# Kernel optimization log

Measured on AMD Instinct MI355X. Metric: run time of the kernel, lower is better.

The kernel has to match this reference:

```python
import jax, jax.numpy as jnp
import numpy as np

B, L, D, H, V, NBARS = 128, 256, 256, 256, 130, 17


def _lstm(x, h, c, Wih, Whh, bih, bhh):
    # torch nn.LSTMCell math
    g = x @ Wih.T + h @ Whh.T + (bih + bhh)
    i, f, gg, o = jnp.split(g, 4, axis=-1)
    c2 = jax.nn.sigmoid(f) * c + jax.nn.sigmoid(i) * jnp.tanh(gg)
    return jax.nn.sigmoid(o) * jnp.tanh(c2), c2


def setup_inputs() -> dict:
    key = jax.random.key(0)
    ks = jax.random.split(key, 10)
    s = 0.05
    return dict(
        c=jax.random.normal(ks[0], (B, NBARS, D), jnp.float32),
        target=jax.random.randint(ks[1], (3, B, L), 0, V),
        length=L,
        W_hid=jax.random.normal(ks[2], (2 * D, D), jnp.float32) * s,
        b_hid=jnp.zeros((2 * D,), jnp.float32),
        W1_ih=jax.random.normal(ks[3], (3, 4 * H, 2 * D), jnp.float32) * s,
        W1_hh=jax.random.normal(ks[4], (3, 4 * H, H), jnp.float32) * s,
        b1_ih=jnp.zeros((3, 4 * H), jnp.float32),
        b1_hh=jnp.zeros((3, 4 * H), jnp.float32),
        Wc_ih=jax.random.normal(ks[5], (4 * H, 3 * H), jnp.float32) * s,
        Wc_hh=jax.random.normal(ks[6], (4 * H, H), jnp.float32) * s,
        bc_ih=jnp.zeros((4 * H,), jnp.float32),
        bc_hh=jnp.zeros((4 * H,), jnp.float32),
        emb=jax.random.normal(ks[7], (3, V, D), jnp.float32) * s,
        Wout=jax.random.normal(ks[8], (3, V, H), jnp.float32) * s,
        bout=jnp.zeros((3, V), jnp.float32),
    )


def _forward(c, W_hid, b_hid, W1_ih, W1_hh, b1_ih, b1_hh, Wc_ih, Wc_hh,
             bc_ih, bc_hh, emb, Wout, bout, target, length):
    Bsz = c.shape[0]
    # initial notes: embedding of token 0 for each of the 3 streams
    notes0 = jnp.broadcast_to(emb[:, 0, :][:, None, :], (3, Bsz, D))
    z3 = jnp.zeros((3, Bsz, H), c.dtype)
    z1 = jnp.zeros((Bsz, H), c.dtype)
    carry0 = (z3, z3, z3, z3, z1, z1, notes0)

    def step(carry, t):
        h1, c1, h2, c2, hc, cc, notes = carry
        bar = t // 16
        c_bar = jax.lax.dynamic_index_in_dim(c, bar, axis=1, keepdims=False)      # [B, D]
        c_t = jax.lax.dynamic_index_in_dim(c, bar + 1, axis=1, keepdims=False)    # [B, D]
        h_init = jnp.tanh(c_bar @ W_hid.T + b_hid)[:, :H]
        reset = (t % 16) == 0
        rs = lambda x: jnp.where(reset, jnp.broadcast_to(h_init, x.shape), x)
        zr = lambda x: jnp.where(reset, jnp.zeros_like(x), x)
        h1, c1, h2, c2, hc, cc = rs(h1), zr(c1), rs(h2), zr(c2), rs(hc), zr(cc)

        # first lstm1 update for all 3 streams (independent -> vmap)
        c_t3 = jnp.broadcast_to(c_t, (3,) + c_t.shape)
        x1 = jnp.concatenate([notes, c_t3], axis=-1)                               # [3, B, 2D]
        h1, c1 = jax.vmap(_lstm)(x1, h1, c1, W1_ih, W1_hh, b1_ih, b1_hh)

        tgt = jax.lax.dynamic_index_in_dim(target, t, axis=2, keepdims=False)      # [3, B]
        h1l = [h1[i] for i in range(3)]
        c1l = [c1[i] for i in range(3)]
        h2l = [h2[i] for i in range(3)]
        c2l = [c2[i] for i in range(3)]
        nl = [notes[i] for i in range(3)]
        outs = []
        # sequential dependency through the context cell -> small fixed loop of 3
        for i in range(3):
            hc, cc = _lstm(jnp.concatenate(h1l, axis=-1), hc, cc, Wc_ih, Wc_hh, bc_ih, bc_hh)
            h2l[i], c2l[i] = _lstm(jnp.concatenate([hc, c_t], axis=-1), h2l[i], c2l[i],
                                   W1_ih[i], W1_hh[i], b1_ih[i], b1_hh[i])
            outs.append((h1l[i] + h2l[i]) @ Wout[i].T + bout[i])                   # [B, V]
            nl[i] = emb[i][tgt[i]]                                                 # teacher forcing
            h1l[i], c1l[i] = _lstm(jnp.concatenate([nl[i], c_t], axis=-1), h1l[i], c1l[i],
                                   W1_ih[i], W1_hh[i], b1_ih[i], b1_hh[i])
        carry = (jnp.stack(h1l), jnp.stack(c1l), jnp.stack(h2l), jnp.stack(c2l),
                 hc, cc, jnp.stack(nl))
        return carry, jnp.stack(outs)                                              # [3, B, V]

    _, ys = jax.lax.scan(step, carry0, jnp.arange(length))                         # [L, 3, B, V]
    return jnp.transpose(ys, (1, 2, 0, 3))                                         # [3, B, L, V]


def reference(c, target, length, W_hid, b_hid, W1_ih, W1_hh, b1_ih, b1_hh,
              Wc_ih, Wc_hh, bc_ih, bc_hh, emb, Wout, bout):
    return _forward(c, W_hid, b_hid, W1_ih, W1_hh, b1_ih, b1_hh, Wc_ih, Wc_hh,
                    bc_ih, bc_hh, emb, Wout, bout, target, length)
```

## Files before the change

### kernel.cpp

```cpp
#include <hip/hip_runtime.h>
#include <hip/hip_bf16.h>

typedef float  f32x4  __attribute__((ext_vector_type(4)));
typedef short  short8 __attribute__((ext_vector_type(8)));
typedef short  bf4    __attribute__((ext_vector_type(4)));

#define MFMA16(a,b,c) __builtin_amdgcn_mfma_f32_16x16x32_bf16((a),(b),(c),0,0,0)

__device__ __forceinline__ short tobf(float f){
  unsigned u = __float_as_uint(f);
  u += 0x7fffu + ((u >> 16) & 1u);
  return (short)(u >> 16);
}
__device__ __forceinline__ float frombf(short s){
  return __uint_as_float(((unsigned)(unsigned short)s) << 16);
}
__device__ __forceinline__ float sigf(float x){
  return 1.f / (1.f + __expf(-x));
}
__device__ __forceinline__ float tanhf_(float x){
  float ax = fabsf(x);
  float e  = __expf(-2.f * ax);
  float t  = (1.f - e) / (1.f + e);
  return x >= 0.f ? t : -t;
}
__device__ __forceinline__ bf4 pack4(f32x4 v){
  bf4 r; r[0]=tobf(v[0]); r[1]=tobf(v[1]); r[2]=tobf(v[2]); r[3]=tobf(v[3]); return r;
}

__device__ __forceinline__ int hoff(int row, int col){
  return (row*512 + col*2) ^ ((row & 7) << 4);
}
__device__ __forceinline__ void stH(short* buf, int row, int col, short v){
  *(short*)((char*)buf + hoff(row,col)) = v;
}
__device__ __forceinline__ short8 ldA(const short* buf, int k0, int lane){
  int row = lane & 15;
  int off = (row*512 + (k0 + ((lane>>4)<<3))*2) ^ ((row & 7) << 4);
  return *(const short8*)((const char*)buf + off);
}
__device__ __forceinline__ short* cpPtr(short* cp, int s, int w, int g, int lane){
  return cp + (((s*16 + w)*4 + g) << 8) + (lane << 2);
}
__device__ __forceinline__ f32x4 ldCP(const short* cp, int s, int w, int g, int lane){
  bf4 v = *(const bf4*)(cp + (((s*16 + w)*4 + g) << 8) + (lane << 2));
  f32x4 r; r[0]=frombf(v[0]); r[1]=frombf(v[1]); r[2]=frombf(v[2]); r[3]=frombf(v[3]);
  return r;
}
__device__ __forceinline__ f32x4 ldCS(const float* b, int sl, int tid){
  return *(const f32x4*)(b + sl*4096 + tid*4);
}
__device__ __forceinline__ void stCS(float* b, int sl, int tid, f32x4 v){
  *(f32x4*)(b + sl*4096 + tid*4) = v;
}

__device__ __forceinline__ void gemm256(f32x4 (&acc)[4], const short* __restrict__ W,
                                        int KT, int kt0, const short* __restrict__ A,
                                        int lane, int w){
  const short* w0 = W + (((     w)*KT + kt0)*64 + lane)*8;
  const short* w1 = W + (((16 + w)*KT + kt0)*64 + lane)*8;
  const short* w2 = W + (((32 + w)*KT + kt0)*64 + lane)*8;
  const short* w3 = W + (((48 + w)*KT + kt0)*64 + lane)*8;
  short8 b0[4], b1[4], b2[4], b3[4];
#define GLD(B,K) do{ (B)[0]=*(const short8*)(w0+(K)*512); (B)[1]=*(const short8*)(w1+(K)*512); \
                     (B)[2]=*(const short8*)(w2+(K)*512); (B)[3]=*(const short8*)(w3+(K)*512);}while(0)
#define GMM(B,K) do{ short8 a0_=ldA(A,(K)*32,lane); \
  acc[0]=MFMA16(a0_,(B)[0],acc[0]); acc[1]=MFMA16(a0_,(B)[1],acc[1]); \
  acc[2]=MFMA16(a0_,(B)[2],acc[2]); acc[3]=MFMA16(a0_,(B)[3],acc[3]);}while(0)
  GLD(b0,0); GLD(b1,1); GLD(b2,2); GLD(b3,3);
  GMM(b0,0); GLD(b0,4);
  GMM(b1,1); GLD(b1,5);
  GMM(b2,2); GLD(b2,6);
  GMM(b3,3); GLD(b3,7);
  GMM(b0,4);
  GMM(b1,5);
  GMM(b2,6);
  GMM(b3,7);
#undef GLD
#undef GMM
}

__device__ __forceinline__ void gemm256_dual(f32x4 (&acc)[4], f32x4 (&dacc)[4],
                                             const short* __restrict__ W,
                                             const short* __restrict__ A1,
                                             const short* __restrict__ A2,
                                             int lane, int w){
  const short* w0 = W + ((     w)*8*64 + lane)*8;
  const short* w1 = W + ((16 + w)*8*64 + lane)*8;
  const short* w2 = W + ((32 + w)*8*64 + lane)*8;
  const short* w3 = W + ((48 + w)*8*64 + lane)*8;
  short8 b0[4], b1[4];
#define DLD2(B,K) do{ (B)[0]=*(const short8*)(w0+(K)*512); (B)[1]=*(const short8*)(w1+(K)*512); \
                      (B)[2]=*(const short8*)(w2+(K)*512); (B)[3]=*(const short8*)(w3+(K)*512);}while(0)
#define DMM2(B,K) do{ short8 a1_=ldA(A1,(K)*32,lane); short8 a2_=ldA(A2,(K)*32,lane); \
  acc[0]=MFMA16(a1_,(B)[0],acc[0]);  dacc[0]=MFMA16(a2_,(B)[0],dacc[0]); \
  acc[1]=MFMA16(a1_,(B)[1],acc[1]);  dacc[1]=MFMA16(a2_,(B)[1],dacc[1]); \
  acc[2]=MFMA16(a1_,(B)[2],acc[2]);  dacc[2]=MFMA16(a2_,(B)[2],dacc[2]); \
  acc[3]=MFMA16(a1_,(B)[3],acc[3]);  dacc[3]=MFMA16(a2_,(B)[3],dacc[3]);}while(0)
  DLD2(b0,0); DLD2(b1,1);
  DMM2(b0,0); DLD2(b0,2);
  DMM2(b1,1); DLD2(b1,3);
  DMM2(b0,2); DLD2(b0,4);
  DMM2(b1,3); DLD2(b1,5);
  DMM2(b0,4); DLD2(b0,6);
  DMM2(b1,5); DLD2(b1,7);
  DMM2(b0,6);
  DMM2(b1,7);
#undef DLD2
#undef DMM2
}

__global__ void swz_kernel(short* __restrict__ dst, const float* __restrict__ src,
                           int rowStride, int colOff, int Nreal,
                           int KTtot, int kt0, int ktN, int NT){
  int idx = blockIdx.x*256 + threadIdx.x;
  if (idx >= NT*ktN*512) return;
  int j = idx & 7, l = (idx>>3) & 63, tile = idx >> 9;
  int nt = tile / ktN, ktl = tile - nt*ktN;
  int n = nt*16 + (l & 15);
  int k = ktl*32 + ((l>>4)<<3) + j;
  float v = (n < Nreal) ? src[n*rowStride + colOff + k] : 0.f;
  dst[(((nt*KTtot + kt0 + ktl)*64 + l)<<3) + j] = tobf(v);
}

__global__ __launch_bounds__(1024) void eproj_kernel(
    const float* __restrict__ emb, const float* __restrict__ b1_ih,
    const float* __restrict__ b1_hh, const short* __restrict__ W1ihA_s,
    short* __restrict__ eprojb){
  __shared__ short es[36864];
  const int s = blockIdx.x;
  const int tid = threadIdx.x, lane = tid & 63, w = tid >> 6;
  const int l15 = lane & 15, lg = lane >> 4;
  for (int idx = tid; idx < 36864; idx += 1024){
    int row = idx >> 8, c2 = idx & 255;
    float v = (row < 130) ? emb[(s*130 + row)*256 + c2] : 0.f;
    *(short*)((char*)es + ((row*512 + c2*2) ^ ((row & 7) << 4))) = tobf(v);
  }
  __syncthreads();
  f32x4 z4 = {0.f,0.f,0.f,0.f};
  for (int rt = 0; rt < 9; ++rt){
    const short* Arow = es + rt*4096;
    f32x4 acc[4] = {z4, z4, z4, z4};
    #pragma unroll 2
    for (int kt = 0; kt < 8; ++kt){
      short8 a = ldA(Arow, kt*32, lane);
      #pragma unroll
      for (int q = 0; q < 4; ++q){
        short8 b = *(const short8*)(W1ihA_s + s*262144 + (((w*4+q)*8 + kt)*64 + lane)*8);
        acc[q] = MFMA16(a, b, acc[q]);
      }
    }
    #pragma unroll
    for (int q = 0; q < 4; ++q)
      #pragma unroll
      for (int r = 0; r < 4; ++r){
        int v = rt*16 + lg*4 + r;
        if (v < 130){
          int gc = (w*4 + q)*16 + l15;
          eprojb[(s*130 + v)*1024 + ((gc & 255) << 2) + (gc >> 8)] =
            tobf(acc[q][r] + b1_ih[s*1024 + gc] + b1_hh[s*1024 + gc]);
        }
      }
  }
}

__global__ __launch_bounds__(1024)
__attribute__((amdgpu_waves_per_eu(4,4))) void rnn_main(
    const float* __restrict__ cbuf, const int* __restrict__ tgt,
    const float* __restrict__ b_hid, const float* __restrict__ b1_ih,
    const float* __restrict__ b1_hh, const float* __restrict__ bc_ih,
    const float* __restrict__ bc_hh, const float* __restrict__ boutp,
    const short* __restrict__ eprojb, short* __restrict__ cpart,
    float* __restrict__ cst,
    const short* __restrict__ W1hh_s, const short* __restrict__ W1ihA_s,
    const short* __restrict__ W1ihB_s, const short* __restrict__ Wc_s,
    const short* __restrict__ Whid_s, const short* __restrict__ Wout_s,
    float* __restrict__ outp)
{
  __shared__ short h1b[3*4096];
  __shared__ short h2b[3*4096];
  __shared__ short hcb[4096];

  const int tid  = threadIdx.x;
  const int lane = tid & 63;
  const int w    = tid >> 6;
  const int l15  = lane & 15;
  const int lg   = lane >> 4;
  const int chunk = blockIdx.x;
  const int bar   = blockIdx.y;
  const int b0    = chunk * 16;
  const int cc    = w*16 + l15;
  const int wgid  = bar*8 + chunk;

  short* cpWG  = cpart + wgid*49152;
  float* cstWG = cst + (size_t)wgid*28672;
  const f32x4 z4 = {0.f,0.f,0.f,0.f};

  #pragma unroll 1
  for (int tt = 0; tt < 16; ++tt){
    const int t = bar*16 + tt;

    if (tt == 0){
      for (int idx = tid; idx < 4096; idx += 1024){
        int row = idx >> 8, c2 = idx & 255;
        stH(h2b,        row, c2, tobf(cbuf[((b0+row)*17 + bar)*256 + c2]));
        stH(h2b + 4096, row, c2, tobf(cbuf[((b0+row)*17 + bar + 1)*256 + c2]));
      }
      __syncthreads();
      f32x4 hi0 = z4;
      #pragma unroll
      for (int kt = 0; kt < 8; ++kt){
        short8 a0 = ldA(h2b, kt*32, lane);
        short8 bb = *(const short8*)(Whid_s + ((w*8 + kt)*64 + lane)*8);
        hi0 = MFMA16(a0, bb, hi0);
      }
      #pragma unroll 1
      for (int s = 0; s < 3; ++s){
        f32x4 acc[4] = {z4, z4, z4, z4};
        gemm256(acc, W1ihB_s + s*262144, 8, 0, h2b + 4096, lane, w);
        #pragma unroll
        for (int g = 0; g < 4; ++g)
          *(bf4*)cpPtr(cpWG, s, w, g, lane) = pack4(acc[g]);
      }
      __syncthreads();
      {
        float bh = b_hid[cc];
        #pragma unroll
        for (int r = 0; r < 4; ++r){
          int row = lg*4 + r;
          short hv = tobf(tanhf_(hi0[r] + bh));
          stH(h1b,       row,cc,hv); stH(h1b+4096, row,cc,hv); stH(h1b+8192,row,cc,hv);
          stH(h2b,       row,cc,hv); stH(h2b+4096, row,cc,hv); stH(h2b+8192,row,cc,hv);
          stH(hcb,       row,cc,hv);
        }
      }
      __syncthreads();
    }

    #pragma unroll 1
    for (int s = 0; s < 3; ++s){
      f32x4 cold = tt ? ldCS(cstWG, s, tid) : z4;
      f32x4 acc[4];
      #pragma unroll
      for (int g = 0; g < 4; ++g) acc[g] = ldCP(cpWG, s, w, g, lane);
      gemm256(acc, W1hh_s + s*262144, 8, 0, h1b + s*4096, lane, w);
      __syncthreads();
      f32x4 cnew;
      #pragma unroll
      for (int r = 0; r < 4; ++r){
        const int row = lg*4 + r;
        const int tok = (t == 0) ? 0 : tgt[(s*128 + b0 + row)*256 + (t-1)];
        bf4 e4 = *(const bf4*)(eprojb + (size_t)(s*130 + tok)*1024 + cc*4);
        float pi = acc[0][r] + frombf(e4[0]);
        float pf = acc[1][r] + frombf(e4[1]);
        float pg = acc[2][r] + frombf(e4[2]);
        float po = acc[3][r] + frombf(e4[3]);
        float cs = sigf(pf)*cold[r] + sigf(pi)*tanhf_(pg);
        cnew[r] = cs;
        stH(h1b + s*4096, row, cc, tobf(sigf(po)*tanhf_(cs)));
      }
      stCS(cstWG, s, tid, cnew);
    }
    __syncthreads();

    #pragma unroll 1
    for (int i = 0; i < 3; ++i){
      {
        f32x4 cold = (tt == 0 && i == 0) ? z4 : ldCS(cstWG, 6, tid);
        f32x4 acc[4] = {z4, z4, z4, z4};
        #pragma unroll 1
        for (int seg = 0; seg < 4; ++seg){
          const short* Ax = (seg==0) ? h1b : (seg==1) ? (h1b+4096)
                           : (seg==2) ? (h1b+8192) : hcb;
          gemm256(acc, Wc_s, 32, seg*8, Ax, lane, w);
        }
        __syncthreads();
        const float bi = bc_ih[cc]      + bc_hh[cc];
        const float bf = bc_ih[256+cc]  + bc_hh[256+cc];
        const float bg = bc_ih[512+cc]  + bc_hh[512+cc];
        const float bo = bc_ih[768+cc]  + bc_hh[768+cc];
        f32x4 cnew;
        #pragma unroll
        for (int r = 0; r < 4; ++r){
          const int row = lg*4 + r;
          float cs = sigf(acc[1][r] + bf)*cold[r]
                   + sigf(acc[0][r] + bi)*tanhf_(acc[2][r] + bg);
          cnew[r] = cs;
          stH(hcb, row, cc, tobf(sigf(acc[3][r] + bo)*tanhf_(cs)));
        }
        stCS(cstWG, 6, tid, cnew);
        __syncthreads();
      }
      f32x4 dacc[4];
      {
        f32x4 cold = (tt == 0) ? z4 : ldCS(cstWG, 3+i, tid);
        f32x4 acc[4];
        #pragma unroll
        for (int g = 0; g < 4; ++g){ acc[g] = ldCP(cpWG, i, w, g, lane); dacc[g] = acc[g]; }
        gemm256(acc, W1ihA_s + i*262144, 8, 0, hcb, lane, w);
        gemm256_dual(acc, dacc, W1hh_s + i*262144, h2b + i*4096, h1b + i*4096, lane, w);
        __syncthreads();
        const float bi = b1_ih[i*1024+cc]      + b1_hh[i*1024+cc];
        const float bf = b1_ih[i*1024+256+cc]  + b1_hh[i*1024+256+cc];
        const float bg = b1_ih[i*1024+512+cc]  + b1_hh[i*1024+512+cc];
        const float bo = b1_ih[i*1024+768+cc]  + b1_hh[i*1024+768+cc];
        f32x4 cnew;
        #pragma unroll
        for (int r = 0; r < 4; ++r){
          const int row = lg*4 + r;
          float cs = sigf(acc[1][r] + bf)*cold[r]
                   + sigf(acc[0][r] + bi)*tanhf_(acc[2][r] + bg);
          cnew[r] = cs;
          stH(h2b + i*4096, row, cc, tobf(sigf(acc[3][r] + bo)*tanhf_(cs)));
        }
        stCS(cstWG, 3+i, tid, cnew);
        __syncthreads();
      }
      {
        f32x4 cold = ldCS(cstWG, i, tid);
        f32x4 e0 = z4;
        const short* h1p = h1b + i*4096;
        const short* h2p = h2b + i*4096;
        if (w < 9){
          const short* wo = Wout_s + i*36864 + ((w*8)*64 + lane)*8;
          short8 ebA = *(const short8*)(wo);
          short8 ebB = *(const short8*)(wo + 512);
#define EMM(EB,K) do{ short8 a_=ldA(h1p,(K)*32,lane), f_=ldA(h2p,(K)*32,lane); \
  e0 = MFMA16(a_,(EB),e0); e0 = MFMA16(f_,(EB),e0); }while(0)
          EMM(ebA,0); ebA = *(const short8*)(wo + 2*512);
          EMM(ebB,1); ebB = *(const short8*)(wo + 3*512);
          EMM(ebA,2); ebA = *(const short8*)(wo + 4*512);
          EMM(ebB,3); ebB = *(const short8*)(wo + 5*512);
          EMM(ebA,4); ebA = *(const short8*)(wo + 6*512);
          EMM(ebB,5); ebB = *(const short8*)(wo + 7*512);
          EMM(ebA,6);
          EMM(ebB,7);
#undef EMM
        }
        __syncthreads();
        f32x4 cnew;
        #pragma unroll
        for (int r = 0; r < 4; ++r){
          const int row = lg*4 + r;
          const int tok = tgt[(i*128 + b0 + row)*256 + t];
          bf4 e4 = *(const bf4*)(eprojb + (size_t)(i*130 + tok)*1024 + cc*4);
          float pi = dacc[0][r] + frombf(e4[0]);
          float pf = dacc[1][r] + frombf(e4[1]);
          float pg = dacc[2][r] + frombf(e4[2]);
          float po = dacc[3][r] + frombf(e4[3]);
          float cs = sigf(pf)*cold[r] + sigf(pi)*tanhf_(pg);
          cnew[r] = cs;
          stH(h1b + i*4096, row, cc, tobf(sigf(po)*tanhf_(cs)));
        }
        stCS(cstWG, i, tid, cnew);
        if (w < 8){
          const int v = w*16 + l15;
          const float bo = boutp[i*130 + v];
          #pragma unroll
          for (int r = 0; r < 4; ++r){
            const int row = lg*4 + r;
            outp[(size_t)((i*128 + b0 + row)*256 + t)*130 + v] = e0[r] + bo;
          }
        } else if (w == 8 && l15 < 2){
          const int v = 128 + l15;
          const float bo = boutp[i*130 + v];
          #pragma unroll
          for (int r = 0; r < 4; ++r){
            const int row = lg*4 + r;
            outp[(size_t)((i*128 + b0 + row)*256 + t)*130 + v] = e0[r] + bo;
          }
        }
        __syncthreads();
      }
    }
  }
}

extern "C" void kernel_launch(void* const* d_in, const int* in_sizes, int n_in,
                              void* d_out, int out_size, void* d_ws, size_t ws_size,
                              hipStream_t stream){
  (void)in_sizes; (void)n_in; (void)out_size; (void)ws_size;
  const float* c     = (const float*)d_in[0];
  const int*   tgt   = (const int*)  d_in[1];
  const float* W_hid = (const float*)d_in[3];
  const float* b_hid = (const float*)d_in[4];
  const float* W1_ih = (const float*)d_in[5];
  const float* W1_hh = (const float*)d_in[6];
  const float* b1_ih = (const float*)d_in[7];
  const float* b1_hh = (const float*)d_in[8];
  const float* Wc_ih = (const float*)d_in[9];
  const float* Wc_hh = (const float*)d_in[10];
  const float* bc_ih = (const float*)d_in[11];
  const float* bc_hh = (const float*)d_in[12];
  const float* emb   = (const float*)d_in[13];
  const float* Wout  = (const float*)d_in[14];
  const float* bout  = (const float*)d_in[15];
  float* outp = (float*)d_out;

  short* ws = (short*)d_ws;
  short* W1hh_s  = ws;
  short* W1ihA_s = ws + 786432;
  short* W1ihB_s = ws + 1572864;
  short* Wc_s    = ws + 2359296;
  short* Whid_s  = ws + 3407872;
  short* Wout_s  = ws + 3473408;
  short* eprojb  = ws + 3584000;
  short* cpart   = ws + 3983360;
  float* cstate  = (float*)((char*)d_ws + 20549632);

  for (int s = 0; s < 3; ++s){
    swz_kernel<<<1024,256,0,stream>>>(W1hh_s  + s*262144, W1_hh + s*262144, 256,   0, 1024,  8, 0,  8, 64);
    swz_kernel<<<1024,256,0,stream>>>(W1ihA_s + s*262144, W1_ih + s*524288, 512,   0, 1024,  8, 0,  8, 64);
    swz_kernel<<<1024,256,0,stream>>>(W1ihB_s + s*262144, W1_ih + s*524288, 512, 256, 1024,  8, 0,  8, 64);
    swz_kernel<<< 144,256,0,stream>>>(Wout_s  + s*36864,  Wout  + s*33280,  256,   0,  130,  8, 0,  8,  9);
  }
  swz_kernel<<<3072,256,0,stream>>>(Wc_s,   Wc_ih, 768, 0, 1024, 32,  0, 24, 64);
  swz_kernel<<<1024,256,0,stream>>>(Wc_s,   Wc_hh, 256, 0, 1024, 32, 24,  8, 64);
  swz_kernel<<< 256,256,0,stream>>>(Whid_s, W_hid, 256, 0,  512,  8,  0,  8, 16);
  eproj_kernel<<<3,1024,0,stream>>>(emb, b1_ih, b1_hh, W1ihA_s, eprojb);

  rnn_main<<<dim3(8,16),1024,0,stream>>>(c, tgt, b_hid, b1_ih, b1_hh, bc_ih, bc_hh,
                                         bout, eprojb, cpart, cstate,
                                         W1hh_s, W1ihA_s, W1ihB_s,
                                         Wc_s, Whid_s, Wout_s, outp);
}
```

Baseline: 2.747 ms.

## Stream GEMM weight tiles through LDS with global_load_lds triple buffering

Replaces direct global-to-register weight loads in the recurrent GEMMs with asynchronous global_load_lds transfers into a triple-buffered shared-memory staging area, using manual vmcnt waits. Each wave then reads its weight fragments from LDS. The aim is deeper, asynchronous prefetch of weights with less register pressure. It adds 96KB of LDS, and the hand-written vmcnt counting can interact badly with other outstanding loads.

```diff
diff --git a/kernel.cpp b/kernel.cpp
--- a/kernel.cpp
+++ b/kernel.cpp
@@ -6,6 +6,9 @@
 typedef short  bf4    __attribute__((ext_vector_type(4)));
 
 #define MFMA16(a,b,c) __builtin_amdgcn_mfma_f32_16x16x32_bf16((a),(b),(c),0,0,0)
+#define GLOADLDS(SRC, DST) __builtin_amdgcn_global_load_lds( \
+  (const __attribute__((address_space(1))) void*)(SRC), \
+  (__attribute__((address_space(3))) void*)(DST), 16, 0, 0)
 
 __device__ __forceinline__ short tobf(float f){
   unsigned u = __float_as_uint(f);
@@ -80,34 +83,63 @@
 #undef GMM
 }
 
-__device__ __forceinline__ void gemm256_dual(f32x4 (&acc)[4], f32x4 (&dacc)[4],
-                                             const short* __restrict__ W,
-                                             const short* __restrict__ A1,
-                                             const short* __restrict__ A2,
-                                             int lane, int w){
-  const short* w0 = W + ((     w)*8*64 + lane)*8;
-  const short* w1 = W + ((16 + w)*8*64 + lane)*8;
-  const short* w2 = W + ((32 + w)*8*64 + lane)*8;
-  const short* w3 = W + ((48 + w)*8*64 + lane)*8;
-  short8 b0[4], b1[4];
-#define DLD2(B,K) do{ (B)[0]=*(const short8*)(w0+(K)*512); (B)[1]=*(const short8*)(w1+(K)*512); \
-                      (B)[2]=*(const short8*)(w2+(K)*512); (B)[3]=*(const short8*)(w3+(K)*512);}while(0)
-#define DMM2(B,K) do{ short8 a1_=ldA(A1,(K)*32,lane); short8 a2_=ldA(A2,(K)*32,lane); \
-  acc[0]=MFMA16(a1_,(B)[0],acc[0]);  dacc[0]=MFMA16(a2_,(B)[0],dacc[0]); \
-  acc[1]=MFMA16(a1_,(B)[1],acc[1]);  dacc[1]=MFMA16(a2_,(B)[1],dacc[1]); \
-  acc[2]=MFMA16(a1_,(B)[2],acc[2]);  dacc[2]=MFMA16(a2_,(B)[2],dacc[2]); \
-  acc[3]=MFMA16(a1_,(B)[3],acc[3]);  dacc[3]=MFMA16(a2_,(B)[3],dacc[3]);}while(0)
-  DLD2(b0,0); DLD2(b1,1);
-  DMM2(b0,0); DLD2(b0,2);
-  DMM2(b1,1); DLD2(b1,3);
-  DMM2(b0,2); DLD2(b0,4);
-  DMM2(b1,3); DLD2(b1,5);
-  DMM2(b0,4); DLD2(b0,6);
-  DMM2(b1,5); DLD2(b1,7);
-  DMM2(b0,6);
-  DMM2(b1,7);
-#undef DLD2
-#undef DMM2
+#define HST(B,H) do{ \
+    const int kt_ = kt0 + ((H)>>1); \
+    const int gb_ = ((H)&1)<<1; \
+    GLOADLDS(Wb + ((((gb_    )*16 + w)*KT + kt_) << 9) + (lane<<3), \
+             (char*)wb + (B)*32768 + (w<<11)); \
+    GLOADLDS(Wb + ((((gb_ + 1)*16 + w)*KT + kt_) << 9) + (lane<<3), \
+             (char*)wb + (B)*32768 + (w<<11) + 1024); \
+  }while(0)
+#define WAITH(H) do{ \
+    if ((H) < 14)      { asm volatile("s_waitcnt vmcnt(4)" ::: "memory"); } \
+    else if ((H) == 14){ asm volatile("s_waitcnt vmcnt(2)" ::: "memory"); } \
+    else               { asm volatile("s_waitcnt vmcnt(0)" ::: "memory"); } \
+    __builtin_amdgcn_sched_barrier(0); \
+  }while(0)
+
+__device__ __forceinline__ void gemmL(f32x4 (&acc)[4], const short* __restrict__ Wb,
+                                      int KT, int kt0, const short* __restrict__ A,
+                                      short* wb, int lane, int w){
+  HST(0,0); HST(1,1); HST(2,2);
+  #pragma unroll
+  for (int h = 0; h < 16; ++h){
+    WAITH(h);
+    const int b = h % 3;
+    const char* base = (const char*)wb + b*32768 + (w<<11) + (lane<<4);
+    short8 t0 = *(const short8*)(base);
+    short8 t1 = *(const short8*)(base + 1024);
+    short8 a0_ = ldA(A, (h>>1)*32, lane);
+    const int g0 = (h&1)<<1;
+    acc[g0]   = MFMA16(a0_, t0, acc[g0]);
+    acc[g0+1] = MFMA16(a0_, t1, acc[g0+1]);
+    if (h < 13) HST((h+3)%3, h+3);
+  }
+}
+
+__device__ __forceinline__ void gemmL_dual(f32x4 (&acc)[4], f32x4 (&dacc)[4],
+                                           const short* __restrict__ Wb,
+                                           const short* __restrict__ A1,
+                                           const short* __restrict__ A2,
+                                           short* wb, int lane, int w){
+  const int KT = 8, kt0 = 0;
+  HST(0,0); HST(1,1); HST(2,2);
+  #pragma unroll
+  for (int h = 0; h < 16; ++h){
+    WAITH(h);
+    const int b = h % 3;
+    const char* base = (const char*)wb + b*32768 + (w<<11) + (lane<<4);
+    short8 t0 = *(const short8*)(base);
+    short8 t1 = *(const short8*)(base + 1024);
+    short8 a1_ = ldA(A1, (h>>1)*32, lane);
+    short8 a2_ = ldA(A2, (h>>1)*32, lane);
+    const int g0 = (h&1)<<1;
+    acc[g0]    = MFMA16(a1_, t0, acc[g0]);
+    dacc[g0]   = MFMA16(a2_, t0, dacc[g0]);
+    acc[g0+1]  = MFMA16(a1_, t1, acc[g0+1]);
+    dacc[g0+1] = MFMA16(a2_, t1, dacc[g0+1]);
+    if (h < 13) HST((h+3)%3, h+3);
+  }
 }
 
 __global__ void swz_kernel(short* __restrict__ dst, const float* __restrict__ src,
@@ -180,6 +212,7 @@
   __shared__ short h1b[3*4096];
   __shared__ short h2b[3*4096];
   __shared__ short hcb[4096];
+  __shared__ short wbuf[49152];
 
   const int tid  = threadIdx.x;
   const int lane = tid & 63;
@@ -243,7 +276,7 @@
       f32x4 acc[4];
       #pragma unroll
       for (int g = 0; g < 4; ++g) acc[g] = ldCP(cpWG, s, w, g, lane);
-      gemm256(acc, W1hh_s + s*262144, 8, 0, h1b + s*4096, lane, w);
+      gemmL(acc, W1hh_s + s*262144, 8, 0, h1b + s*4096, wbuf, lane, w);
       __syncthreads();
       f32x4 cnew;
       #pragma unroll
@@ -272,7 +305,7 @@
         for (int seg = 0; seg < 4; ++seg){
           const short* Ax = (seg==0) ? h1b : (seg==1) ? (h1b+4096)
                            : (seg==2) ? (h1b+8192) : hcb;
-          gemm256(acc, Wc_s, 32, seg*8, Ax, lane, w);
+          gemmL(acc, Wc_s, 32, seg*8, Ax, wbuf, lane, w);
         }
         __syncthreads();
         const float bi = bc_ih[cc]      + bc_hh[cc];
@@ -297,8 +330,8 @@
         f32x4 acc[4];
         #pragma unroll
         for (int g = 0; g < 4; ++g){ acc[g] = ldCP(cpWG, i, w, g, lane); dacc[g] = acc[g]; }
-        gemm256(acc, W1ihA_s + i*262144, 8, 0, hcb, lane, w);
-        gemm256_dual(acc, dacc, W1hh_s + i*262144, h2b + i*4096, h1b + i*4096, lane, w);
+        gemmL(acc, W1ihA_s + i*262144, 8, 0, hcb, wbuf, lane, w);
+        gemmL_dual(acc, dacc, W1hh_s + i*262144, h2b + i*4096, h1b + i*4096, wbuf, lane, w);
         __syncthreads();
         const float bi = b1_ih[i*1024+cc]      + b1_hh[i*1024+cc];
         const float bf = b1_ih[i*1024+256+cc]  + b1_hh[i*1024+256+cc];
```

Result: faster. 2.644 ms, median of 3 (-3.7%).

## Stream LSTM weights through LDS with async global_load_lds double buffering

Applied to the files above, without the earlier changes.

Replaces the direct register weight loads in the W1hh, Wc and fused W1ihA/W1hh GEMMs with a pipe2 helper. It issues global_load_lds copies into a double-buffered 64KB LDS region and waits on vmcnt before each consumer step, so weight fetches overlap the MFMAs. Per-bar context partial products now stay in registers as packed bf16 instead of going through a global scratch buffer, and the Wc cell state moves from global memory to shared memory. The cost is higher LDS usage, which may limit occupancy at 1024 threads, and more register pressure from the twelve held bf4 values.

```diff
diff --git a/kernel.cpp b/kernel.cpp
--- a/kernel.cpp
+++ b/kernel.cpp
@@ -6,6 +6,9 @@
 typedef short  bf4    __attribute__((ext_vector_type(4)));
 
 #define MFMA16(a,b,c) __builtin_amdgcn_mfma_f32_16x16x32_bf16((a),(b),(c),0,0,0)
+#define GLOADLDS(SRC, DST) __builtin_amdgcn_global_load_lds( \
+  (const __attribute__((address_space(1))) void*)(SRC), \
+  (__attribute__((address_space(3))) void*)(DST), 16, 0, 0)
 
 __device__ __forceinline__ short tobf(float f){
   unsigned u = __float_as_uint(f);
@@ -27,6 +30,10 @@
 __device__ __forceinline__ bf4 pack4(f32x4 v){
   bf4 r; r[0]=tobf(v[0]); r[1]=tobf(v[1]); r[2]=tobf(v[2]); r[3]=tobf(v[3]); return r;
 }
+__device__ __forceinline__ f32x4 unpack4(bf4 v){
+  f32x4 r; r[0]=frombf(v[0]); r[1]=frombf(v[1]); r[2]=frombf(v[2]); r[3]=frombf(v[3]);
+  return r;
+}
 
 __device__ __forceinline__ int hoff(int row, int col){
   return (row*512 + col*2) ^ ((row & 7) << 4);
@@ -38,14 +45,6 @@
   int row = lane & 15;
   int off = (row*512 + (k0 + ((lane>>4)<<3))*2) ^ ((row & 7) << 4);
   return *(const short8*)((const char*)buf + off);
-}
-__device__ __forceinline__ short* cpPtr(short* cp, int s, int w, int g, int lane){
-  return cp + (((s*16 + w)*4 + g) << 8) + (lane << 2);
-}
-__device__ __forceinline__ f32x4 ldCP(const short* cp, int s, int w, int g, int lane){
-  bf4 v = *(const bf4*)(cp + (((s*16 + w)*4 + g) << 8) + (lane << 2));
-  f32x4 r; r[0]=frombf(v[0]); r[1]=frombf(v[1]); r[2]=frombf(v[2]); r[3]=frombf(v[3]);
-  return r;
 }
 __device__ __forceinline__ f32x4 ldCS(const float* b, int sl, int tid){
   return *(const f32x4*)(b + sl*4096 + tid*4);
@@ -80,34 +79,24 @@
 #undef GMM
 }
 
-__device__ __forceinline__ void gemm256_dual(f32x4 (&acc)[4], f32x4 (&dacc)[4],
-                                             const short* __restrict__ W,
-                                             const short* __restrict__ A1,
-                                             const short* __restrict__ A2,
-                                             int lane, int w){
-  const short* w0 = W + ((     w)*8*64 + lane)*8;
-  const short* w1 = W + ((16 + w)*8*64 + lane)*8;
-  const short* w2 = W + ((32 + w)*8*64 + lane)*8;
-  const short* w3 = W + ((48 + w)*8*64 + lane)*8;
-  short8 b0[4], b1[4];
-#define DLD2(B,K) do{ (B)[0]=*(const short8*)(w0+(K)*512); (B)[1]=*(const short8*)(w1+(K)*512); \
-                      (B)[2]=*(const short8*)(w2+(K)*512); (B)[3]=*(const short8*)(w3+(K)*512);}while(0)
-#define DMM2(B,K) do{ short8 a1_=ldA(A1,(K)*32,lane); short8 a2_=ldA(A2,(K)*32,lane); \
-  acc[0]=MFMA16(a1_,(B)[0],acc[0]);  dacc[0]=MFMA16(a2_,(B)[0],dacc[0]); \
-  acc[1]=MFMA16(a1_,(B)[1],acc[1]);  dacc[1]=MFMA16(a2_,(B)[1],dacc[1]); \
-  acc[2]=MFMA16(a1_,(B)[2],acc[2]);  dacc[2]=MFMA16(a2_,(B)[2],dacc[2]); \
-  acc[3]=MFMA16(a1_,(B)[3],acc[3]);  dacc[3]=MFMA16(a2_,(B)[3],dacc[3]);}while(0)
-  DLD2(b0,0); DLD2(b1,1);
-  DMM2(b0,0); DLD2(b0,2);
-  DMM2(b1,1); DLD2(b1,3);
-  DMM2(b0,2); DLD2(b0,4);
-  DMM2(b1,3); DLD2(b1,5);
-  DMM2(b0,4); DLD2(b0,6);
-  DMM2(b1,5); DLD2(b1,7);
-  DMM2(b0,6);
-  DMM2(b1,7);
-#undef DLD2
-#undef DMM2
+template<int NH, class FS, class FC>
+__device__ __forceinline__ void pipe2(FS fsrc, FC fcons, short* wb, int w, int lane){
+#define STG(B,H) do{ \
+    GLOADLDS(fsrc((H),0) + (lane<<3), (char*)wb + (B)*32768 + (w<<11)); \
+    GLOADLDS(fsrc((H),1) + (lane<<3), (char*)wb + (B)*32768 + (w<<11) + 1024); }while(0)
+  STG(0,0); STG(1,1);
+  #pragma unroll
+  for (int h = 0; h < NH; ++h){
+    if (h < NH-1) asm volatile("s_waitcnt vmcnt(2)" ::: "memory");
+    else          asm volatile("s_waitcnt vmcnt(0)" ::: "memory");
+    __builtin_amdgcn_sched_barrier(0);
+    const char* base = (const char*)wb + (h&1)*32768 + (w<<11) + (lane<<4);
+    short8 t0 = *(const short8*)(base);
+    short8 t1 = *(const short8*)(base + 1024);
+    fcons(h, t0, t1);
+    if (h + 2 < NH) STG(h&1, h+2);
+  }
+#undef STG
 }
 
 __global__ void swz_kernel(short* __restrict__ dst, const float* __restrict__ src,
@@ -170,7 +159,7 @@
     const float* __restrict__ b_hid, const float* __restrict__ b1_ih,
     const float* __restrict__ b1_hh, const float* __restrict__ bc_ih,
     const float* __restrict__ bc_hh, const float* __restrict__ boutp,
-    const short* __restrict__ eprojb, short* __restrict__ cpart,
+    const short* __restrict__ eprojb,
     float* __restrict__ cst,
     const short* __restrict__ W1hh_s, const short* __restrict__ W1ihA_s,
     const short* __restrict__ W1ihB_s, const short* __restrict__ Wc_s,
@@ -180,6 +169,8 @@
   __shared__ short h1b[3*4096];
   __shared__ short h2b[3*4096];
   __shared__ short hcb[4096];
+  __shared__ float ccb[4096];
+  __shared__ short wbuf[32768];
 
   const int tid  = threadIdx.x;
   const int lane = tid & 63;
@@ -192,9 +183,10 @@
   const int cc    = w*16 + l15;
   const int wgid  = bar*8 + chunk;
 
-  short* cpWG  = cpart + wgid*49152;
   float* cstWG = cst + (size_t)wgid*28672;
   const f32x4 z4 = {0.f,0.f,0.f,0.f};
+
+  bf4 c00,c01,c02,c03, c10,c11,c12,c13, c20,c21,c22,c23;
 
   #pragma unroll 1
   for (int tt = 0; tt < 16; ++tt){
@@ -214,13 +206,13 @@
         short8 bb = *(const short8*)(Whid_s + ((w*8 + kt)*64 + lane)*8);
         hi0 = MFMA16(a0, bb, hi0);
       }
-      #pragma unroll 1
+      #pragma unroll
       for (int s = 0; s < 3; ++s){
         f32x4 acc[4] = {z4, z4, z4, z4};
         gemm256(acc, W1ihB_s + s*262144, 8, 0, h2b + 4096, lane, w);
-        #pragma unroll
-        for (int g = 0; g < 4; ++g)
-          *(bf4*)cpPtr(cpWG, s, w, g, lane) = pack4(acc[g]);
+        if (s == 0){ c00=pack4(acc[0]); c01=pack4(acc[1]); c02=pack4(acc[2]); c03=pack4(acc[3]); }
+        else if (s == 1){ c10=pack4(acc[0]); c11=pack4(acc[1]); c12=pack4(acc[2]); c13=pack4(acc[3]); }
+        else { c20=pack4(acc[0]); c21=pack4(acc[1]); c22=pack4(acc[2]); c23=pack4(acc[3]); }
       }
       __syncthreads();
       {
@@ -240,10 +232,24 @@
     #pragma unroll 1
     for (int s = 0; s < 3; ++s){
       f32x4 cold = tt ? ldCS(cstWG, s, tid) : z4;
-      f32x4 acc[4];
-      #pragma unroll
-      for (int g = 0; g < 4; ++g) acc[g] = ldCP(cpWG, s, w, g, lane);
-      gemm256(acc, W1hh_s + s*262144, 8, 0, h1b + s*4096, lane, w);
+      bf4 cp0,cp1,cp2,cp3;
+      if (s == 0){ cp0=c00; cp1=c01; cp2=c02; cp3=c03; }
+      else if (s == 1){ cp0=c10; cp1=c11; cp2=c12; cp3=c13; }
+      else { cp0=c20; cp1=c21; cp2=c22; cp3=c23; }
+      f32x4 acc[4] = { unpack4(cp0), unpack4(cp1), unpack4(cp2), unpack4(cp3) };
+      const short* Wp = W1hh_s + s*262144;
+      const short* hs = h1b + s*4096;
+      pipe2<16>(
+        [&](int h, int j)->const short*{
+          const int kt = h>>1, g = ((h&1)<<1) + j;
+          return Wp + (((g*16 + w)*8 + kt) << 9);
+        },
+        [&](int h, short8 t0, short8 t1){
+          short8 a0_ = ldA(hs, (h>>1)*32, lane);
+          const int g0 = (h&1)<<1;
+          acc[g0]   = MFMA16(a0_, t0, acc[g0]);
+          acc[g0+1] = MFMA16(a0_, t1, acc[g0+1]);
+        }, wbuf, w, lane);
       __syncthreads();
       f32x4 cnew;
       #pragma unroll
@@ -265,15 +271,27 @@
 
     #pragma unroll 1
     for (int i = 0; i < 3; ++i){
+      bf4 cpi0,cpi1,cpi2,cpi3;
+      if (i == 0){ cpi0=c00; cpi1=c01; cpi2=c02; cpi3=c03; }
+      else if (i == 1){ cpi0=c10; cpi1=c11; cpi2=c12; cpi3=c13; }
+      else { cpi0=c20; cpi1=c21; cpi2=c22; cpi3=c23; }
       {
-        f32x4 cold = (tt == 0 && i == 0) ? z4 : ldCS(cstWG, 6, tid);
+        f32x4 cold = (tt == 0 && i == 0) ? z4 : *(const f32x4*)(ccb + tid*4);
         f32x4 acc[4] = {z4, z4, z4, z4};
-        #pragma unroll 1
-        for (int seg = 0; seg < 4; ++seg){
-          const short* Ax = (seg==0) ? h1b : (seg==1) ? (h1b+4096)
-                           : (seg==2) ? (h1b+8192) : hcb;
-          gemm256(acc, Wc_s, 32, seg*8, Ax, lane, w);
-        }
+        pipe2<64>(
+          [&](int h, int j)->const short*{
+            const int kt = h>>1, g = ((h&1)<<1) + j;
+            return Wc_s + (((g*16 + w)*32 + kt) << 9);
+          },
+          [&](int h, short8 t0, short8 t1){
+            const int kt = h>>1;
+            const short* Ax = (kt<8) ? h1b : (kt<16) ? (h1b+4096)
+                             : (kt<24) ? (h1b+8192) : hcb;
+            short8 a0_ = ldA(Ax, (kt&7)*32, lane);
+            const int g0 = (h&1)<<1;
+            acc[g0]   = MFMA16(a0_, t0, acc[g0]);
+            acc[g0+1] = MFMA16(a0_, t1, acc[g0+1]);
+          }, wbuf, w, lane);
         __syncthreads();
         const float bi = bc_ih[cc]      + bc_hh[cc];
         const float bf = bc_ih[256+cc]  + bc_hh[256+cc];
@@ -288,17 +306,42 @@
           cnew[r] = cs;
           stH(hcb, row, cc, tobf(sigf(acc[3][r] + bo)*tanhf_(cs)));
         }
-        stCS(cstWG, 6, tid, cnew);
+        *(f32x4*)(ccb + tid*4) = cnew;
         __syncthreads();
       }
       f32x4 dacc[4];
       {
         f32x4 cold = (tt == 0) ? z4 : ldCS(cstWG, 3+i, tid);
-        f32x4 acc[4];
-        #pragma unroll
-        for (int g = 0; g < 4; ++g){ acc[g] = ldCP(cpWG, i, w, g, lane); dacc[g] = acc[g]; }
-        gemm256(acc, W1ihA_s + i*262144, 8, 0, hcb, lane, w);
-        gemm256_dual(acc, dacc, W1hh_s + i*262144, h2b + i*4096, h1b + i*4096, lane, w);
+        f32x4 acc[4] = { unpack4(cpi0), unpack4(cpi1), unpack4(cpi2), unpack4(cpi3) };
+        dacc[0]=acc[0]; dacc[1]=acc[1]; dacc[2]=acc[2]; dacc[3]=acc[3];
+        const short* WA = W1ihA_s + i*262144;
+        const short* WH = W1hh_s  + i*262144;
+        const short* h1p = h1b + i*4096;
+        const short* h2p = h2b + i*4096;
+        pipe2<32>(
+          [&](int h, int j)->const short*{
+            if (h < 16){ const int kt=h>>1, g=((h&1)<<1)+j;
+                         return WA + (((g*16 + w)*8 + kt) << 9); }
+            const int hh=h-16, kt=hh>>1, g=((hh&1)<<1)+j;
+            return WH + (((g*16 + w)*8 + kt) << 9);
+          },
+          [&](int h, short8 t0, short8 t1){
+            if (h < 16){
+              short8 a0_ = ldA(hcb, (h>>1)*32, lane);
+              const int g0 = (h&1)<<1;
+              acc[g0]   = MFMA16(a0_, t0, acc[g0]);
+              acc[g0+1] = MFMA16(a0_, t1, acc[g0+1]);
+            } else {
+              const int hh = h-16;
+              short8 a1_ = ldA(h2p, (hh>>1)*32, lane);
+              short8 a2_ = ldA(h1p, (hh>>1)*32, lane);
+              const int g0 = (hh&1)<<1;
+              acc[g0]    = MFMA16(a1_, t0, acc[g0]);
+              dacc[g0]   = MFMA16(a2_, t0, dacc[g0]);
+              acc[g0+1]  = MFMA16(a1_, t1, acc[g0+1]);
+              dacc[g0+1] = MFMA16(a2_, t1, dacc[g0+1]);
+            }
+          }, wbuf, w, lane);
         __syncthreads();
         const float bi = b1_ih[i*1024+cc]      + b1_hh[i*1024+cc];
         const float bf = b1_ih[i*1024+256+cc]  + b1_hh[i*1024+256+cc];
@@ -405,7 +448,6 @@
   short* Whid_s  = ws + 3407872;
   short* Wout_s  = ws + 3473408;
   short* eprojb  = ws + 3584000;
-  short* cpart   = ws + 3983360;
   float* cstate  = (float*)((char*)d_ws + 20549632);
 
   for (int s = 0; s < 3; ++s){
@@ -420,7 +462,7 @@
   eproj_kernel<<<3,1024,0,stream>>>(emb, b1_ih, b1_hh, W1ihA_s, eprojb);
 
   rnn_main<<<dim3(8,16),1024,0,stream>>>(c, tgt, b_hid, b1_ih, b1_hh, bc_ih, bc_hh,
-                                         bout, eprojb, cpart, cstate,
+                                         bout, eprojb, cstate,
                                          W1hh_s, W1ihA_s, W1ihB_s,
                                          Wc_s, Whid_s, Wout_s, outp);
 }
```

Result: slower. 7.345 ms (+167.4%).
